# Optimization experiments

Measured on AMD Instinct MI355X. Metric: run time of the kernel, lower is better.

The kernel has to match this reference:

```python
import jax, jax.numpy as jnp
import numpy as np

B, N, D, K, L, H, DFF = 2048, 64, 256, 32, 2, 8, 1024
TEMP = 10.0
EPS = 1e-10


def _ln(x, g, b):
    m = jnp.mean(x, -1, keepdims=True)
    v = jnp.mean((x - m) ** 2, -1, keepdims=True)
    return (x - m) * jax.lax.rsqrt(v + 1e-5) * g + b


def _mha(x, Wqkv, bqkv, Wo, bo):
    b, n, d = x.shape
    dh = d // H
    qkv = x @ Wqkv.T + bqkv                      # [b,n,3d]
    q, k, v = jnp.split(qkv, 3, axis=-1)
    q = q.reshape(b, n, H, dh)
    k = k.reshape(b, n, H, dh)
    v = v.reshape(b, n, H, dh)
    att = jnp.einsum('bqhd,bkhd->bhqk', q, k) / np.float32(np.sqrt(dh))
    att = jax.nn.softmax(att, axis=-1)
    o = jnp.einsum('bhqk,bkhd->bqhd', att, v).reshape(b, n, d)
    return o @ Wo.T + bo


def _encoder(x, Wqkv, bqkv, Wo, bo, ln1_g, ln1_b, ln2_g, ln2_b, W1, b1, W2, b2):
    # torch TransformerEncoder, norm_first=False (post-LN), dropout=0
    for l in range(L):
        x = _ln(x + _mha(x, Wqkv[l], bqkv[l], Wo[l], bo[l]), ln1_g[l], ln1_b[l])
        h = jax.nn.relu(x @ W1[l].T + b1[l]) @ W2[l].T + b2[l]
        x = _ln(x + h, ln2_g[l], ln2_b[l])
    return x


def _cluster_probs_from_emb(emb, mus):
    # ||x - tanh(mu)||^2 via expansion to avoid the [B,N,K,D] intermediate
    mt = jnp.tanh(mus)                                       # [K,D]
    d2 = (jnp.sum(emb ** 2, -1)[..., None]
          - 2.0 * jnp.einsum('bnd,kd->bnk', emb, mt)
          + jnp.sum(mt ** 2, -1))                            # [B,N,K]
    e = jnp.exp(-d2 / TEMP)
    return e / jnp.sum(e, -1, keepdims=True)


def _forward(input_series, init_logits, transition_logits,
             Wqkv, bqkv, Wo, bo, ln1_g, ln1_b, ln2_g, ln2_b,
             W1, b1, W2, b2, mus):
    prob_pi = jax.nn.softmax(init_logits, axis=0)            # [K]
    prob_A = jax.nn.softmax(transition_logits, axis=1)       # [K,K]
    emb_all = _encoder(input_series, Wqkv, bqkv, Wo, bo,
                       ln1_g, ln1_b, ln2_g, ln2_b, W1, b1, W2, b2)
    logits_all = _cluster_probs_from_emb(emb_all, mus)       # [B,N,K]

    log_emit = jnp.log(logits_all + EPS)                     # [B,N,K]
    lt0 = jax.nn.softmax(jnp.log(prob_pi + EPS)[None, :] + log_emit[:, 0], axis=1)

    def step(lt, le):
        lt = jax.nn.softmax(jnp.log(lt @ prob_A + EPS) + le, axis=1)
        return lt, lt

    _, rest = jax.lax.scan(step, lt0, jnp.swapaxes(log_emit[:, 1:], 0, 1))
    cluster_probs = jnp.concatenate([lt0[:, None], jnp.swapaxes(rest, 0, 1)], axis=1)
    entropy_loss = -jnp.mean(jnp.sum(cluster_probs * jnp.log(cluster_probs + EPS), -1))
    return cluster_probs, emb_all, prob_pi, prob_A, entropy_loss


def setup_inputs() -> dict:
    key = jax.random.key(0)
    ks = jax.random.split(key, 10)
    s = jnp.float32(0.02)
    return {
        'input_series': jax.random.normal(ks[0], (B, N, D), jnp.float32),
        'init_logits': jax.random.normal(ks[1], (K,), jnp.float32),
        'transition_logits': jax.random.normal(ks[2], (K, K), jnp.float32),
        'Wqkv': jax.random.normal(ks[3], (L, 3 * D, D), jnp.float32) * s,
        'bqkv': jnp.zeros((L, 3 * D), jnp.float32),
        'Wo': jax.random.normal(ks[4], (L, D, D), jnp.float32) * s,
        'bo': jnp.zeros((L, D), jnp.float32),
        'ln1_g': jnp.ones((L, D), jnp.float32),
        'ln1_b': jnp.zeros((L, D), jnp.float32),
        'ln2_g': jnp.ones((L, D), jnp.float32),
        'ln2_b': jnp.zeros((L, D), jnp.float32),
        'W1': jax.random.normal(ks[5], (L, DFF, D), jnp.float32) * s,
        'b1': jnp.zeros((L, DFF), jnp.float32),
        'W2': jax.random.normal(ks[6], (L, D, DFF), jnp.float32) * s,
        'b2': jnp.zeros((L, D), jnp.float32),
        'mus': jax.random.normal(ks[7], (K, D), jnp.float32),
    }


def reference(input_series, init_logits, transition_logits, Wqkv, bqkv, Wo, bo,
              ln1_g, ln1_b, ln2_g, ln2_b, W1, b1, W2, b2, mus):
    return _forward(input_series, init_logits, transition_logits, Wqkv, bqkv,
                    Wo, bo, ln1_g, ln1_b, ln2_g, ln2_b, W1, b1, W2, b2, mus)
```

## Files before the change

kernel.cpp:

```cpp
#include <hip/hip_runtime.h>

#define BB   2048
#define NNX  64
#define DD   256
#define KKC  32
#define LLN  2
#define HHN  8
#define DHH  32
#define DFFN 1024
#define BNT  (BB*NNX)

typedef short s16x8 __attribute__((ext_vector_type(8)));
typedef float f32x4 __attribute__((ext_vector_type(4)));

#define GLOAD_LDS16(gp, lp) __builtin_amdgcn_global_load_lds( \
    (const __attribute__((address_space(1))) void*)(gp),      \
    (__attribute__((address_space(3))) void*)(lp), 16, 0, 0)

#define WAITVM4() asm volatile("s_waitcnt vmcnt(4)" ::: "memory")
#define WAITVM0() asm volatile("s_waitcnt vmcnt(0)" ::: "memory")
#define WAITLGKM0() do { asm volatile("s_waitcnt lgkmcnt(0)" ::: "memory"); \
                         __builtin_amdgcn_sched_barrier(0); } while (0)
#define SBAR() __builtin_amdgcn_s_barrier()

__device__ __forceinline__ unsigned short f2bf(float f) {
  unsigned int u = __float_as_uint(f);
  u += 0x7fffu + ((u >> 16) & 1u);
  return (unsigned short)(u >> 16);
}
__device__ __forceinline__ float bf2f(unsigned short u) {
  return __uint_as_float(((unsigned int)u) << 16);
}

__device__ __forceinline__ unsigned char f2fp8(float f) {
  unsigned u = __float_as_uint(f);
  unsigned lsb = (u >> 20) & 1u;
  u += 0x7FFFFu + lsb;
  int e = (int)((u >> 23) & 255u) - 120;
  if (e <= 0) {
    int q = (int)(f * 512.f + 0.5f);
    return (unsigned char)q;
  }
  if (e > 15) return 0x7E;
  return (unsigned char)((e << 3) | ((u >> 20) & 7u));
}
__device__ __forceinline__ unsigned char f2fp8s(float f) {
  unsigned s = __float_as_uint(f) >> 31;
  float a = fminf(fabsf(f), 448.f);
  return (unsigned char)((s << 7) | f2fp8(a));
}
__device__ __forceinline__ unsigned char p2fp8(float f) {
  unsigned u = __float_as_uint(f);
  u += 0x7FFFFu + ((u >> 20) & 1u);
  int e = (int)((u >> 23) & 255u) - 120;
  if (e <= 0) return 0;
  return (unsigned char)((e << 3) | ((u >> 20) & 7u));
}

__global__ __launch_bounds__(256) void cvt_kernel(const float4* __restrict__ src,
                                                  ushort4* __restrict__ dst, int n4) {
  int i = blockIdx.x * 256 + threadIdx.x;
  int st = gridDim.x * 256;
  for (; i < n4; i += st) {
    float4 v = src[i];
    ushort4 o;
    o.x = f2bf(v.x); o.y = f2bf(v.y); o.z = f2bf(v.z); o.w = f2bf(v.w);
    dst[i] = o;
  }
}

__global__ __launch_bounds__(256) void cvtw_kernel(const float4* __restrict__ wq, ushort4* __restrict__ dq,
                                                   const float4* __restrict__ wo, ushort4* __restrict__ dov,
                                                   const float4* __restrict__ w1, ushort4* __restrict__ d1,
                                                   const float4* __restrict__ w2, uchar4* __restrict__ d2,
                                                   const float* __restrict__ mus, unsigned short* __restrict__ mtb,
                                                   float* __restrict__ mtn,
                                                   const float* __restrict__ il, const float* __restrict__ tl,
                                                   float* __restrict__ d_pi, float* __restrict__ d_A,
                                                   float* __restrict__ d_ent) {
  if (blockIdx.x >= 512) {
    int lane = threadIdx.x;
    if (blockIdx.x == 512) {
      if (lane < 32) {
        float acc = 0.f;
        for (int d = 0; d < 256; d++) {
          float t = tanhf(mus[lane * 256 + d]);
          mtb[lane * 264 + d] = f2bf(t);
          acc += t * t;
        }
        mtn[lane] = acc;
      }
    } else {
      if (lane == 0) *d_ent = 0.f;
      if (lane < 32) {
        float v = il[lane];
        float mx = v;
        #pragma unroll
        for (int off = 16; off; off >>= 1) mx = fmaxf(mx, __shfl_xor(mx, off, 32));
        float e = expf(v - mx), sm = e;
        #pragma unroll
        for (int off = 16; off; off >>= 1) sm += __shfl_xor(sm, off, 32);
        d_pi[lane] = e / sm;
        for (int r = 0; r < 32; r++) {
          float a = tl[r * 32 + lane];
          float m2 = a;
          #pragma unroll
          for (int off = 16; off; off >>= 1) m2 = fmaxf(m2, __shfl_xor(m2, off, 32));
          float e2 = expf(a - m2), s2 = e2;
          #pragma unroll
          for (int off = 16; off; off >>= 1) s2 += __shfl_xor(s2, off, 32);
          d_A[r * 32 + lane] = e2 / s2;
        }
      }
    }
    return;
  }
  const int n0 = 98304, n1 = 32768, n2 = 131072, n3 = 131072;
  int i = blockIdx.x * 256 + threadIdx.x;
  int st = 512 * 256;
  for (; i < n0 + n1 + n2 + n3; i += st) {
    int j = i;
    if (j < n0) {
      float4 v = wq[j];
      dq[j] = (ushort4){f2bf(v.x), f2bf(v.y), f2bf(v.z), f2bf(v.w)};
    } else if ((j -= n0) < n1) {
      float4 v = wo[j];
      dov[j] = (ushort4){f2bf(v.x), f2bf(v.y), f2bf(v.z), f2bf(v.w)};
    } else if ((j -= n1) < n2) {
      float4 v = w1[j];
      d1[j] = (ushort4){f2bf(v.x), f2bf(v.y), f2bf(v.z), f2bf(v.w)};
    } else {
      j -= n2;
      float4 v = w2[j];
      d2[j] = (uchar4){f2fp8s(v.x * 64.f), f2fp8s(v.y * 64.f),
                       f2fp8s(v.z * 64.f), f2fp8s(v.w * 64.f)};
    }
  }
}

template <int EPI>
__global__ __launch_bounds__(256, 4) void gemm_nt(const unsigned short* __restrict__ A,
                                                  const unsigned short* __restrict__ Bw,
                                                  const float* __restrict__ bias,
                                                  void* __restrict__ outp,
                                                  int N, int K, int nx) {
  __shared__ unsigned short lds[16384];
  const int t = threadIdx.x;
  const int bid = blockIdx.x, nwg = gridDim.x;
  const int wg = (bid & 7) * (nwg >> 3) + (bid >> 3);
  const int m0 = (wg / nx) << 7;
  const int n0 = (wg % nx) << 7;
  const int lane = t & 63, w = t >> 6;
  const int wm = w >> 1, wn = w & 1;
  const int lr = lane & 15, lk = lane >> 4;

  const int r0 = t >> 2, sg = t & 3;
  const int s0 = sg ^ ((r0 >> 1) & 3);
  const int r1 = r0 + 64;
  const int s1 = sg ^ ((r1 >> 1) & 3);
  const int aoff0 = (m0 + r0) * K + s0 * 8;
  const int aoff1 = (m0 + r1) * K + s1 * 8;
  const int boff0 = (n0 + r0) * K + s0 * 8;
  const int boff1 = (n0 + r1) * K + s1 * 8;

#define STAGE(buf, k0) do {                                    \
    char* la = (char*)lds + (buf) * 16384;                     \
    GLOAD_LDS16(A + aoff0 + (k0), la + t * 16);                \
    GLOAD_LDS16(A + aoff1 + (k0), la + 4096 + t * 16);         \
    GLOAD_LDS16(Bw + boff0 + (k0), la + 8192 + t * 16);        \
    GLOAD_LDS16(Bw + boff1 + (k0), la + 12288 + t * 16);       \
  } while (0)

  f32x4 acc[4][4];
  #pragma unroll
  for (int i = 0; i < 4; i++)
    #pragma unroll
    for (int j = 0; j < 4; j++) acc[i][j] = (f32x4)(0.f);

  const int ra = wm * 64 + lr, rb = wn * 64 + lr;
  const int sla = lk ^ ((ra >> 1) & 3), slb = lk ^ ((rb >> 1) & 3);

  const int NT = K >> 5;
  STAGE(0, 0);
  STAGE(1, 32);
  WAITVM4();
  SBAR();

  int c = 0;
  for (int kt = 0; kt < NT; kt++) {
    s16x8 af[4], bf[4];
    {
      const unsigned short* ua = lds + c * 8192;
      const unsigned short* ub = ua + 4096;
      #pragma unroll
      for (int mf = 0; mf < 4; mf++)
        af[mf] = *(const s16x8*)&ua[(ra + mf * 16) * 32 + sla * 8];
      #pragma unroll
      for (int nf = 0; nf < 4; nf++)
        bf[nf] = *(const s16x8*)&ub[(rb + nf * 16) * 32 + slb * 8];
    }
    __builtin_amdgcn_s_setprio(1);
    #pragma unroll
    for (int mf = 0; mf < 4; mf++)
      #pragma unroll
      for (int nf = 0; nf < 4; nf++)
        acc[mf][nf] = __builtin_amdgcn_mfma_f32_16x16x32_bf16(af[mf], bf[nf], acc[mf][nf], 0, 0, 0);
    __builtin_amdgcn_s_setprio(0);
    SBAR();
    if (kt < NT - 2) {
      STAGE(c, (kt + 2) << 5);
      WAITVM4();
    } else if (kt == NT - 2) {
      WAITVM0();
    }
    SBAR();
    c ^= 1;
  }
#undef STAGE

  #pragma unroll
  for (int nf = 0; nf < 4; nf++) {
    int col = n0 + wn * 64 + nf * 16 + lr;
    float bv = bias[col];
    #pragma unroll
    for (int mf = 0; mf < 4; mf++)
      #pragma unroll
      for (int r = 0; r < 4; r++) {
        int row = m0 + wm * 64 + mf * 16 + lk * 4 + r;
        size_t o = (size_t)row * N + col;
        float v = acc[mf][nf][r] + bv;
        if (EPI == 0) {
          ((unsigned short*)outp)[o] = f2bf(v);
        } else if (EPI == 1) {
          float hh = fminf(fmaxf(v, 0.f) * 8.f, 448.f);
          ((unsigned char*)outp)[o] = f2fp8(hh);
        } else {
          ((unsigned char*)outp)[o] = f2fp8s(v * 32.f);
        }
      }
  }
}

template <bool WR32>
__global__ __launch_bounds__(512) void gemm_ln(const unsigned short* __restrict__ A,
                                               const unsigned short* __restrict__ Bw,
                                               const float* __restrict__ bias,
                                               const unsigned short* __restrict__ res,
                                               const float* __restrict__ g,
                                               const float* __restrict__ bta,
                                               unsigned short* __restrict__ xb,
                                               float* __restrict__ x32,
                                               int K) {
  __shared__ unsigned short As[128 * 64];
  __shared__ unsigned short Bs[256 * 64];
  __shared__ float stats[2][128][4];
  const int t = threadIdx.x;
  const int nwg = gridDim.x;
  const int bid = blockIdx.x;
  const int wg = (bid & 7) * (nwg >> 3) + (bid >> 3);
  const int m0 = wg << 7;

  const int lane = t & 63, w = t >> 6;
  const int wm = w >> 2, wn = w & 3;
  const int lr = lane & 15, lk = lane >> 4;

  size_t aoff[2], boff[4];
  #pragma unroll
  for (int p = 0; p < 2; p++) {
    int u = p * 512 + t;
    int row = u >> 3, sp = u & 7;
    int seg = sp ^ (((row >> 2) & 1) << 1);
    aoff[p] = (size_t)(m0 + row) * K + seg * 8;
  }
  #pragma unroll
  for (int p = 0; p < 4; p++) {
    int u = p * 512 + t;
    int row = u >> 3, sp = u & 7;
    int seg = sp ^ (((row >> 2) & 1) << 1);
    boff[p] = (size_t)row * K + seg * 8;
  }

  f32x4 acc[4][4];
  #pragma unroll
  for (int i = 0; i < 4; i++)
    #pragma unroll
    for (int j = 0; j < 4; j++) acc[i][j] = (f32x4)(0.f);

  for (int k0 = 0; k0 < K; k0 += 64) {
    #pragma unroll
    for (int p = 0; p < 2; p++)
      GLOAD_LDS16(A + aoff[p] + k0, (char*)As + (p * 512 + t) * 16);
    #pragma unroll
    for (int p = 0; p < 4; p++)
      GLOAD_LDS16(Bw + boff[p] + k0, (char*)Bs + (p * 512 + t) * 16);
    __syncthreads();
    #pragma unroll
    for (int z = 0; z < 2; z++) {
      s16x8 af[4], bfr[4];
      #pragma unroll
      for (int mf = 0; mf < 4; mf++) {
        int row = wm * 64 + mf * 16 + lr;
        int cc = (z * 4 + lk) ^ (((row >> 2) & 1) << 1);
        af[mf] = *(const s16x8*)&As[row * 64 + cc * 8];
      }
      #pragma unroll
      for (int nf = 0; nf < 4; nf++) {
        int row = wn * 64 + nf * 16 + lr;
        int cc = (z * 4 + lk) ^ (((row >> 2) & 1) << 1);
        bfr[nf] = *(const s16x8*)&Bs[row * 64 + cc * 8];
      }
      #pragma unroll
      for (int mf = 0; mf < 4; mf++)
        #pragma unroll
        for (int nf = 0; nf < 4; nf++)
          acc[mf][nf] = __builtin_amdgcn_mfma_f32_16x16x32_bf16(af[mf], bfr[nf], acc[mf][nf], 0, 0, 0);
    }
    __syncthreads();
  }

  float bv[4];
  #pragma unroll
  for (int nf = 0; nf < 4; nf++) bv[nf] = bias[wn * 64 + nf * 16 + lr];

  #pragma unroll
  for (int mf = 0; mf < 4; mf++) {
    #pragma unroll
    for (int r = 0; r < 4; r++) {
      int grow = m0 + wm * 64 + mf * 16 + lk * 4 + r;
      float s = 0.f, q = 0.f;
      #pragma unroll
      for (int nf = 0; nf < 4; nf++) {
        int col = wn * 64 + nf * 16 + lr;
        float v = acc[mf][nf][r] + bv[nf] + bf2f(res[(size_t)grow * 256 + col]);
        acc[mf][nf][r] = v;
        s += v; q += v * v;
      }
      #pragma unroll
      for (int off = 1; off < 16; off <<= 1) { s += __shfl_xor(s, off); q += __shfl_xor(q, off); }
      if (lr == 0) {
        int lrow = wm * 64 + mf * 16 + lk * 4 + r;
        stats[0][lrow][wn] = s;
        stats[1][lrow][wn] = q;
      }
    }
  }
  __syncthreads();

  float gv[4], bbv[4];
  #pragma unroll
  for (int nf = 0; nf < 4; nf++) {
    int col = wn * 64 + nf * 16 + lr;
    gv[nf] = g[col]; bbv[nf] = bta[col];
  }
  #pragma unroll
  for (int mf = 0; mf < 4; mf++) {
    #pragma unroll
    for (int r = 0; r < 4; r++) {
      int lrow = wm * 64 + mf * 16 + lk * 4 + r;
      int grow = m0 + lrow;
      float s4 = stats[0][lrow][0] + stats[0][lrow][1] + stats[0][lrow][2] + stats[0][lrow][3];
      float q4 = stats[1][lrow][0] + stats[1][lrow][1] + stats[1][lrow][2] + stats[1][lrow][3];
      float mean = s4 * (1.f / 256.f);
      float var = q4 * (1.f / 256.f) - mean * mean;
      float rs = rsqrtf(var + 1e-5f);
      #pragma unroll
      for (int nf = 0; nf < 4; nf++) {
        int col = wn * 64 + nf * 16 + lr;
        float val = (acc[mf][nf][r] - mean) * rs * gv[nf] + bbv[nf];
        xb[(size_t)grow * 256 + col] = f2bf(val);
        if (WR32) x32[(size_t)grow * 256 + col] = val;
      }
    }
  }
}

template <bool WR32>
__global__ __launch_bounds__(512) void gemm_ln_fp8(const unsigned char* __restrict__ A,
                                                   const unsigned char* __restrict__ Bw,
                                                   const float* __restrict__ bias,
                                                   const unsigned short* __restrict__ res,
                                                   const float* __restrict__ g,
                                                   const float* __restrict__ bta,
                                                   unsigned short* __restrict__ xb,
                                                   float* __restrict__ x32,
                                                   int K) {
  __shared__ unsigned char lds8[24576];
  float* stats = (float*)lds8;
  const int t = threadIdx.x;
  const int nwg = gridDim.x;
  const int bid = blockIdx.x;
  const int wg = (bid & 7) * (nwg >> 3) + (bid >> 3);
  const int m0 = wg << 7;

  const int lane = t & 63, w = t >> 6;
  const int wm = w >> 2, wn = w & 3;
  const int lr = lane & 15, lk = lane >> 4;

  const int auu = t >> 8, arow = (t >> 1) & 127, asg = t & 1;
  const size_t aoff = (size_t)(m0 + arow) * K + auu * 32 + asg * 16;
  size_t boff[2];
  #pragma unroll
  for (int p = 0; p < 2; p++) {
    int idx = p * 512 + t;
    int buu = idx >> 9, brow = (idx >> 1) & 255, bsg = idx & 1;
    boff[p] = (size_t)brow * K + buu * 32 + bsg * 16;
  }

  f32x4 acc[4][4];
  #pragma unroll
  for (int i = 0; i < 4; i++)
    #pragma unroll
    for (int j = 0; j < 4; j++) acc[i][j] = (f32x4)(0.f);

  for (int k0 = 0; k0 < K; k0 += 64) {
    GLOAD_LDS16(A + aoff + k0, (char*)lds8 + t * 16);
    GLOAD_LDS16(Bw + boff[0] + k0, (char*)lds8 + 8192 + t * 16);
    GLOAD_LDS16(Bw + boff[1] + k0, (char*)lds8 + 16384 + t * 16);
    __syncthreads();
    #pragma unroll
    for (int kk = 0; kk < 2; kk++) {
      long long af[4], bf[4];
      #pragma unroll
      for (int mf = 0; mf < 4; mf++)
        af[mf] = *(const long long*)&lds8[kk * 4096 + (wm * 64 + mf * 16 + lr) * 32 + lk * 8];
      #pragma unroll
      for (int nf = 0; nf < 4; nf++)
        bf[nf] = *(const long long*)&lds8[8192 + kk * 8192 + (wn * 64 + nf * 16 + lr) * 32 + lk * 8];
      #pragma unroll
      for (int mf = 0; mf < 4; mf++)
        #pragma unroll
        for (int nf = 0; nf < 4; nf++)
          acc[mf][nf] = __builtin_amdgcn_mfma_f32_16x16x32_fp8_fp8(af[mf], bf[nf], acc[mf][nf], 0, 0, 0);
    }
    __syncthreads();
  }

  const float isc = 1.f / 512.f;
  float bv[4];
  #pragma unroll
  for (int nf = 0; nf < 4; nf++) bv[nf] = bias[wn * 64 + nf * 16 + lr];

  #pragma unroll
  for (int mf = 0; mf < 4; mf++) {
    #pragma unroll
    for (int r = 0; r < 4; r++) {
      int grow = m0 + wm * 64 + mf * 16 + lk * 4 + r;
      float s = 0.f, q = 0.f;
      #pragma unroll
      for (int nf = 0; nf < 4; nf++) {
        int col = wn * 64 + nf * 16 + lr;
        float v = acc[mf][nf][r] * isc + bv[nf] + bf2f(res[(size_t)grow * 256 + col]);
        acc[mf][nf][r] = v;
        s += v; q += v * v;
      }
      #pragma unroll
      for (int off = 1; off < 16; off <<= 1) { s += __shfl_xor(s, off); q += __shfl_xor(q, off); }
      if (lr == 0) {
        int lrow = wm * 64 + mf * 16 + lk * 4 + r;
        stats[lrow * 4 + wn] = s;
        stats[512 + lrow * 4 + wn] = q;
      }
    }
  }
  __syncthreads();

  float gv[4], bbv[4];
  #pragma unroll
  for (int nf = 0; nf < 4; nf++) {
    int col = wn * 64 + nf * 16 + lr;
    gv[nf] = g[col]; bbv[nf] = bta[col];
  }
  #pragma unroll
  for (int mf = 0; mf < 4; mf++) {
    #pragma unroll
    for (int r = 0; r < 4; r++) {
      int lrow = wm * 64 + mf * 16 + lk * 4 + r;
      int grow = m0 + lrow;
      float s4 = stats[lrow * 4 + 0] + stats[lrow * 4 + 1] + stats[lrow * 4 + 2] + stats[lrow * 4 + 3];
      float q4 = stats[512 + lrow * 4 + 0] + stats[512 + lrow * 4 + 1]
               + stats[512 + lrow * 4 + 2] + stats[512 + lrow * 4 + 3];
      float mean = s4 * (1.f / 256.f);
      float var = q4 * (1.f / 256.f) - mean * mean;
      float rs = rsqrtf(var + 1e-5f);
      #pragma unroll
      for (int nf = 0; nf < 4; nf++) {
        int col = wn * 64 + nf * 16 + lr;
        float val = (acc[mf][nf][r] - mean) * rs * gv[nf] + bbv[nf];
        xb[(size_t)grow * 256 + col] = f2bf(val);
        if (WR32) x32[(size_t)grow * 256 + col] = val;
      }
    }
  }
}

__global__ __launch_bounds__(256) void attn_kernel(const unsigned char* __restrict__ qkv,
                                                   unsigned short* __restrict__ ob) {
  __shared__ unsigned char al[28672];
  const int wv = threadIdx.x >> 6;
  unsigned char* wb = al + wv * 7168;
  unsigned char* qs = wb;
  unsigned char* ks = wb + 2048;
  unsigned char* vs = wb + 4096;
  unsigned char* vt = wb;
  unsigned char* ps = wb + 2304;
  const int bh = blockIdx.x * 4 + wv;
  const int b = bh >> 3, h = bh & 7;
  const int lane = threadIdx.x & 63;
  const int lr = lane & 15, lk = lane >> 4;

  #pragma unroll
  for (int p = 0; p < 2; p++) {
    int u = lane + p * 64;
    int row = u >> 1, seg = u & 1;
    size_t gb = (size_t)(b * 64 + row) * 768 + h * 32 + seg * 16;
    GLOAD_LDS16(qkv + gb, (char*)wb + u * 16);
    GLOAD_LDS16(qkv + gb + 256, (char*)wb + 2048 + u * 16);
    GLOAD_LDS16(qkv + gb + 512, (char*)wb + 4096 + u * 16);
  }
  __syncthreads();

  long long aq[4], bk[4], vchunk[4];
  #pragma unroll
  for (int mi = 0; mi < 4; mi++)
    aq[mi] = *(const long long*)&qs[(mi * 16 + lr) * 32 + lk * 8];
  #pragma unroll
  for (int nj = 0; nj < 4; nj++)
    bk[nj] = *(const long long*)&ks[(nj * 16 + lr) * 32 + lk * 8];
  const int vrow = lane >> 2, vcs = (lane & 3) * 8;
  #pragma unroll
  for (int q = 0; q < 4; q++)
    vchunk[q] = *(const long long*)&vs[(q * 16 + vrow) * 32 + vcs];
  WAITLGKM0();

  #pragma unroll
  for (int q = 0; q < 4; q++) {
    unsigned long long vv = (unsigned long long)vchunk[q];
    #pragma unroll
    for (int j = 0; j < 8; j++)
      vt[(vcs + j) * 72 + q * 16 + vrow] = (unsigned char)(vv >> (8 * j));
  }

  f32x4 s[4][4];
  #pragma unroll
  for (int i = 0; i < 4; i++)
    #pragma unroll
    for (int j = 0; j < 4; j++) s[i][j] = (f32x4)(0.f);
  #pragma unroll
  for (int mi = 0; mi < 4; mi++)
    #pragma unroll
    for (int nj = 0; nj < 4; nj++)
      s[mi][nj] = __builtin_amdgcn_mfma_f32_16x16x32_fp8_fp8(aq[mi], bk[nj], s[mi][nj], 0, 0, 0);

  const float scale = 0.17677669529663687f / 1024.f;
  #pragma unroll
  for (int mi = 0; mi < 4; mi++) {
    #pragma unroll
    for (int r = 0; r < 4; r++) {
      float t0 = s[mi][0][r] * scale, t1 = s[mi][1][r] * scale;
      float t2 = s[mi][2][r] * scale, t3 = s[mi][3][r] * scale;
      float mx = fmaxf(fmaxf(t0, t1), fmaxf(t2, t3));
      #pragma unroll
      for (int off = 8; off; off >>= 1) mx = fmaxf(mx, __shfl_xor(mx, off, 16));
      float e0 = expf(t0 - mx), e1 = expf(t1 - mx), e2 = expf(t2 - mx), e3 = expf(t3 - mx);
      float sm = e0 + e1 + e2 + e3;
      #pragma unroll
      for (int off = 8; off; off >>= 1) sm += __shfl_xor(sm, off, 16);
      float inv = 128.f / sm;
      int prow = mi * 16 + lk * 4 + r;
      ps[prow * 72 + lr + 0]  = p2fp8(e0 * inv);
      ps[prow * 72 + lr + 16] = p2fp8(e1 * inv);
      ps[prow * 72 + lr + 32] = p2fp8(e2 * inv);
      ps[prow * 72 + lr + 48] = p2fp8(e3 * inv);
    }
  }
  WAITLGKM0();

  f32x4 oacc[4][2];
  #pragma unroll
  for (int i = 0; i < 4; i++) { oacc[i][0] = (f32x4)(0.f); oacc[i][1] = (f32x4)(0.f); }
  #pragma unroll
  for (int kk = 0; kk < 2; kk++) {
    long long bv[2];
    #pragma unroll
    for (int nf = 0; nf < 2; nf++)
      bv[nf] = *(const long long*)&vt[(nf * 16 + lr) * 72 + kk * 32 + lk * 8];
    #pragma unroll
    for (int mi = 0; mi < 4; mi++) {
      long long ap = *(const long long*)&ps[(mi * 16 + lr) * 72 + kk * 32 + lk * 8];
      #pragma unroll
      for (int nf = 0; nf < 2; nf++)
        oacc[mi][nf] = __builtin_amdgcn_mfma_f32_16x16x32_fp8_fp8(ap, bv[nf], oacc[mi][nf], 0, 0, 0);
    }
  }
  const float osc = 1.f / 4096.f;
  #pragma unroll
  for (int mi = 0; mi < 4; mi++)
    #pragma unroll
    for (int nf = 0; nf < 2; nf++)
      #pragma unroll
      for (int r = 0; r < 4; r++) {
        int tok = mi * 16 + lk * 4 + r;
        int c = nf * 16 + lr;
        ob[(size_t)(b * 64 + tok) * 256 + h * 32 + c] = f2bf(oacc[mi][nf][r] * osc);
      }
}

__global__ __launch_bounds__(256) void cluster_scan_kernel(const unsigned short* __restrict__ xb,
                                                           const unsigned short* __restrict__ mtb,
                                                           const float* __restrict__ mtn,
                                                           const float* __restrict__ pi,
                                                           const float* __restrict__ Atr,
                                                           float* __restrict__ cp,
                                                           float* __restrict__ ent) {
  __shared__ unsigned short ms[32 * 264];
  __shared__ float les[4][64][32];
  const int t = threadIdx.x;
  for (int i = t; i < 2112; i += 256)
    ((uint2*)ms)[i] = ((const uint2*)mtb)[i];
  const int lane = t & 63, w = t >> 6;
  const int lr = lane & 15, lk = lane >> 4;
  const float mtn0 = mtn[lr], mtn1 = mtn[16 + lr];
  __syncthreads();

  const size_t tok0 = (size_t)blockIdx.x * 256 + (size_t)w * 64;
  f32x4 s[4][2];
  #pragma unroll
  for (int i = 0; i < 4; i++) { s[i][0] = (f32x4)(0.f); s[i][1] = (f32x4)(0.f); }

  #pragma unroll
  for (int kk = 0; kk < 8; kk++) {
    s16x8 bf0 = *(const s16x8*)&ms[lr * 264 + lk * 8 + kk * 32];
    s16x8 bf1 = *(const s16x8*)&ms[(16 + lr) * 264 + lk * 8 + kk * 32];
    #pragma unroll
    for (int mi = 0; mi < 4; mi++) {
      s16x8 af = *(const s16x8*)&xb[(tok0 + mi * 16 + lr) * 256 + lk * 8 + kk * 32];
      s[mi][0] = __builtin_amdgcn_mfma_f32_16x16x32_bf16(af, bf0, s[mi][0], 0, 0, 0);
      s[mi][1] = __builtin_amdgcn_mfma_f32_16x16x32_bf16(af, bf1, s[mi][1], 0, 0, 0);
    }
  }

  #pragma unroll
  for (int mi = 0; mi < 4; mi++) {
    #pragma unroll
    for (int r = 0; r < 4; r++) {
      float l0 = (2.f * s[mi][0][r] - mtn0) * 0.1f;
      float l1 = (2.f * s[mi][1][r] - mtn1) * 0.1f;
      float mx = fmaxf(l0, l1);
      #pragma unroll
      for (int off = 8; off; off >>= 1) mx = fmaxf(mx, __shfl_xor(mx, off, 16));
      float e0 = expf(l0 - mx), e1 = expf(l1 - mx);
      float sm = e0 + e1;
      #pragma unroll
      for (int off = 8; off; off >>= 1) sm += __shfl_xor(sm, off, 16);
      float inv = 1.f / sm;
      int row = mi * 16 + lk * 4 + r;
      les[w][row][lr]      = logf(e0 * inv + 1e-10f);
      les[w][row][16 + lr] = logf(e1 * inv + 1e-10f);
    }
  }

  if (lane < 32) {
    const int j = lane;
    const int batch = blockIdx.x * 4 + w;
    float regA[32];
    #pragma unroll
    for (int i = 0; i < 32; i++) regA[i] = Atr[i * 32 + j];
    float* cpo = cp + (size_t)batch * 64 * 32;

    float u = logf(pi[j] + 1e-10f) + les[w][0][j];
    float mx = u;
    #pragma unroll
    for (int off = 16; off; off >>= 1) mx = fmaxf(mx, __shfl_xor(mx, off, 32));
    float e = expf(u - mx), sm = e;
    #pragma unroll
    for (int off = 16; off; off >>= 1) sm += __shfl_xor(sm, off, 32);
    float p = e / sm;
    cpo[j] = p;
    float enta = p * logf(p + 1e-10f);

    for (int n = 1; n < 64; n++) {
      float tt = 0.f;
      #pragma unroll
      for (int i = 0; i < 32; i++) tt += __shfl(p, i, 32) * regA[i];
      u = logf(tt + 1e-10f) + les[w][n][j];
      mx = u;
      #pragma unroll
      for (int off = 16; off; off >>= 1) mx = fmaxf(mx, __shfl_xor(mx, off, 32));
      e = expf(u - mx); sm = e;
      #pragma unroll
      for (int off = 16; off; off >>= 1) sm += __shfl_xor(sm, off, 32);
      p = e / sm;
      cpo[n * 32 + j] = p;
      enta += p * logf(p + 1e-10f);
    }
    #pragma unroll
    for (int off = 16; off; off >>= 1) enta += __shfl_xor(enta, off, 32);
    if (j == 0) atomicAdd(ent, -enta * (1.f / (2048.f * 64.f)));
  }
}

extern "C" void kernel_launch(void* const* d_in, const int* in_sizes, int n_in,
                              void* d_out, int out_size, void* d_ws, size_t ws_size,
                              hipStream_t stream) {
  const float* input = (const float*)d_in[0];
  const float* init_logits = (const float*)d_in[1];
  const float* trans = (const float*)d_in[2];
  const float* Wqkv = (const float*)d_in[3];
  const float* bqkv = (const float*)d_in[4];
  const float* Wo = (const float*)d_in[5];
  const float* bo = (const float*)d_in[6];
  const float* ln1g = (const float*)d_in[7];
  const float* ln1b = (const float*)d_in[8];
  const float* ln2g = (const float*)d_in[9];
  const float* ln2b = (const float*)d_in[10];
  const float* W1 = (const float*)d_in[11];
  const float* b1 = (const float*)d_in[12];
  const float* W2 = (const float*)d_in[13];
  const float* b2 = (const float*)d_in[14];
  const float* mus = (const float*)d_in[15];

  float* out = (float*)d_out;
  float* cp = out;
  float* x = out + 4194304;
  float* d_pi = out + 37748736;
  float* d_A = out + 37748768;
  float* d_ent = out + 37749792;

  char* ws = (char*)d_ws;
  unsigned char* qkv = (unsigned char*)ws;
  unsigned char* hb = (unsigned char*)ws;
  unsigned short* ob = (unsigned short*)(ws + 268435456ull);
  unsigned short* xb = (unsigned short*)(ws + 335544320ull);
  unsigned short* wq_b = (unsigned short*)(ws + 402653184ull);
  unsigned short* wo_b = (unsigned short*)(ws + 402653184ull + 786432ull);
  unsigned short* w1_b = (unsigned short*)(ws + 402653184ull + 1048576ull);
  unsigned char* w2_f = (unsigned char*)(ws + 402653184ull + 2097152ull);
  unsigned short* mtb = (unsigned short*)(ws + 402653184ull + 3145728ull);
  float* mtn = (float*)(ws + 402653184ull + 3178496ull);

  cvt_kernel<<<2048, 256, 0, stream>>>((const float4*)input, (ushort4*)xb, BNT * 256 / 4);
  cvtw_kernel<<<514, 256, 0, stream>>>((const float4*)Wqkv, (ushort4*)wq_b,
                                       (const float4*)Wo, (ushort4*)wo_b,
                                       (const float4*)W1, (ushort4*)w1_b,
                                       (const float4*)W2, (uchar4*)w2_f,
                                       mus, mtb, mtn,
                                       init_logits, trans, d_pi, d_A, d_ent);

  for (int l = 0; l < 2; l++) {
    gemm_nt<2><<<6144, 256, 0, stream>>>(xb, wq_b + l * 196608, bqkv + l * 768,
                                         qkv, 768, 256, 6);
    attn_kernel<<<4096, 256, 0, stream>>>(qkv, ob);
    gemm_ln<false><<<1024, 512, 0, stream>>>(ob, wo_b + l * 65536, bo + l * 256,
                                             xb, ln1g + l * 256, ln1b + l * 256,
                                             xb, nullptr, 256);
    gemm_nt<1><<<8192, 256, 0, stream>>>(xb, w1_b + l * 262144, b1 + l * 1024,
                                         hb, 1024, 256, 8);
    if (l == LLN - 1)
      gemm_ln_fp8<true><<<1024, 512, 0, stream>>>(hb, w2_f + l * 262144, b2 + l * 256,
                                                  xb, ln2g + l * 256, ln2b + l * 256,
                                                  xb, x, 1024);
    else
      gemm_ln_fp8<false><<<1024, 512, 0, stream>>>(hb, w2_f + l * 262144, b2 + l * 256,
                                                   xb, ln2g + l * 256, ln2b + l * 256,
                                                   xb, nullptr, 1024);
  }

  cluster_scan_kernel<<<512, 256, 0, stream>>>(xb, mtb, mtn, d_pi, d_A, cp, d_ent);
}
```

Measured before the change: 1.060 ms.

## Fuse FFN up and down projections into one fp8 kernel with LayerNorm

Combines the W1 GEMM, ReLU, W2 GEMM and the second LayerNorm into a single kernel. The 64-row hidden chunks stay in shared memory instead of being written to and read back from global memory. W1 and the post-attention activations are now quantized to scaled fp8, so the first GEMM also runs on fp8 MFMA, and gemm_ln writes an extra fp8 copy of x. The fused loop reloads the weights for each chunk with a full wait and barrier and has no double buffering, so memory latency is exposed, and the extra fp8 quantization lowers accuracy.

```diff
diff --git a/kernel.cpp b/kernel.cpp
--- a/kernel.cpp
+++ b/kernel.cpp
@@ -71,7 +71,7 @@
 
 __global__ __launch_bounds__(256) void cvtw_kernel(const float4* __restrict__ wq, ushort4* __restrict__ dq,
                                                    const float4* __restrict__ wo, ushort4* __restrict__ dov,
-                                                   const float4* __restrict__ w1, ushort4* __restrict__ d1,
+                                                   const float4* __restrict__ w1, uchar4* __restrict__ d1,
                                                    const float4* __restrict__ w2, uchar4* __restrict__ d2,
                                                    const float* __restrict__ mus, unsigned short* __restrict__ mtb,
                                                    float* __restrict__ mtn,
@@ -128,7 +128,8 @@
       dov[j] = (ushort4){f2bf(v.x), f2bf(v.y), f2bf(v.z), f2bf(v.w)};
     } else if ((j -= n1) < n2) {
       float4 v = w1[j];
-      d1[j] = (ushort4){f2bf(v.x), f2bf(v.y), f2bf(v.z), f2bf(v.w)};
+      d1[j] = (uchar4){f2fp8s(v.x * 64.f), f2fp8s(v.y * 64.f),
+                       f2fp8s(v.z * 64.f), f2fp8s(v.w * 64.f)};
     } else {
       j -= n2;
       float4 v = w2[j];
@@ -231,9 +232,6 @@
         float v = acc[mf][nf][r] + bv;
         if (EPI == 0) {
           ((unsigned short*)outp)[o] = f2bf(v);
-        } else if (EPI == 1) {
-          float hh = fminf(fmaxf(v, 0.f) * 8.f, 448.f);
-          ((unsigned char*)outp)[o] = f2fp8(hh);
         } else {
           ((unsigned char*)outp)[o] = f2fp8s(v * 32.f);
         }
@@ -241,7 +239,6 @@
   }
 }
 
-template <bool WR32>
 __global__ __launch_bounds__(512) void gemm_ln(const unsigned short* __restrict__ A,
                                                const unsigned short* __restrict__ Bw,
                                                const float* __restrict__ bias,
@@ -249,7 +246,7 @@
                                                const float* __restrict__ g,
                                                const float* __restrict__ bta,
                                                unsigned short* __restrict__ xb,
-                                               float* __restrict__ x32,
+                                               unsigned char* __restrict__ xb8,
                                                int K) {
   __shared__ unsigned short As[128 * 64];
   __shared__ unsigned short Bs[256 * 64];
@@ -367,44 +364,63 @@
       for (int nf = 0; nf < 4; nf++) {
         int col = wn * 64 + nf * 16 + lr;
         float val = (acc[mf][nf][r] - mean) * rs * gv[nf] + bbv[nf];
-        xb[(size_t)grow * 256 + col] = f2bf(val);
-        if (WR32) x32[(size_t)grow * 256 + col] = val;
+        size_t o = (size_t)grow * 256 + col;
+        xb[o] = f2bf(val);
+        xb8[o] = f2fp8s(val * 32.f);
       }
     }
   }
 }
 
 template <bool WR32>
-__global__ __launch_bounds__(512) void gemm_ln_fp8(const unsigned char* __restrict__ A,
-                                                   const unsigned char* __restrict__ Bw,
-                                                   const float* __restrict__ bias,
+__global__ __launch_bounds__(256, 2) void gemm_ffn(const unsigned char* __restrict__ x8,
+                                                   const unsigned char* __restrict__ w1f,
+                                                   const unsigned char* __restrict__ w2f,
+                                                   const float* __restrict__ b1,
+                                                   const float* __restrict__ b2,
                                                    const unsigned short* __restrict__ res,
                                                    const float* __restrict__ g,
                                                    const float* __restrict__ bta,
                                                    unsigned short* __restrict__ xb,
-                                                   float* __restrict__ x32,
-                                                   int K) {
-  __shared__ unsigned char lds8[24576];
+                                                   float* __restrict__ x32) {
+  __shared__ unsigned char lds8[53760];
   float* stats = (float*)lds8;
   const int t = threadIdx.x;
-  const int nwg = gridDim.x;
-  const int bid = blockIdx.x;
+  const int bid = blockIdx.x, nwg = gridDim.x;
   const int wg = (bid & 7) * (nwg >> 3) + (bid >> 3);
-  const int m0 = wg << 7;
-
-  const int lane = t & 63, w = t >> 6;
-  const int wm = w >> 2, wn = w & 3;
+  const int m0 = wg << 6;
+  const int lane = t & 63, wv = t >> 6;
   const int lr = lane & 15, lk = lane >> 4;
 
-  const int auu = t >> 8, arow = (t >> 1) & 127, asg = t & 1;
-  const size_t aoff = (size_t)(m0 + arow) * K + auu * 32 + asg * 16;
-  size_t boff[2];
-  #pragma unroll
-  for (int p = 0; p < 2; p++) {
-    int idx = p * 512 + t;
-    int buu = idx >> 9, brow = (idx >> 1) & 255, bsg = idx & 1;
-    boff[p] = (size_t)brow * K + buu * 32 + bsg * 16;
-  }
+  const int xu = t >> 7, xrow = (t >> 1) & 63, xsg = t & 1;
+
+  #pragma unroll
+  for (int p = 0; p < 4; p++) {
+    int idx = p * 256 + t;
+    int u = idx >> 7, row = (idx >> 1) & 63, sgg = idx & 1;
+    GLOAD_LDS16(x8 + (size_t)(m0 + row) * 256 + u * 32 + sgg * 16, (char*)lds8 + idx * 16);
+  }
+
+#define STAGE_W(c) do {                                                          \
+    _Pragma("unroll")                                                            \
+    for (int p = 0; p < 4; p++) {                                                \
+      int idx = p * 256 + t;                                                     \
+      int u = idx >> 7, row = (idx >> 1) & 63, sgg = idx & 1;                    \
+      GLOAD_LDS16(w1f + (size_t)((c) * 64 + row) * 256 + u * 32 + sgg * 16,      \
+                  (char*)lds8 + 16384 + idx * 16);                               \
+    }                                                                            \
+    _Pragma("unroll")                                                            \
+    for (int p = 0; p < 4; p++) {                                                \
+      int idx = p * 256 + t;                                                     \
+      int u = idx >> 9, row = (idx >> 1) & 255, sgg = idx & 1;                   \
+      GLOAD_LDS16(w2f + (size_t)row * 1024 + (c) * 64 + u * 32 + sgg * 16,       \
+                  (char*)lds8 + 32768 + idx * 16);                               \
+    }                                                                            \
+  } while (0)
+
+  STAGE_W(0);
+  WAITVM0();
+  SBAR();
 
   f32x4 acc[4][4];
   #pragma unroll
@@ -412,54 +428,77 @@
     #pragma unroll
     for (int j = 0; j < 4; j++) acc[i][j] = (f32x4)(0.f);
 
-  for (int k0 = 0; k0 < K; k0 += 64) {
-    GLOAD_LDS16(A + aoff + k0, (char*)lds8 + t * 16);
-    GLOAD_LDS16(Bw + boff[0] + k0, (char*)lds8 + 8192 + t * 16);
-    GLOAD_LDS16(Bw + boff[1] + k0, (char*)lds8 + 16384 + t * 16);
-    __syncthreads();
-    #pragma unroll
-    for (int kk = 0; kk < 2; kk++) {
-      long long af[4], bf[4];
-      #pragma unroll
-      for (int mf = 0; mf < 4; mf++)
-        af[mf] = *(const long long*)&lds8[kk * 4096 + (wm * 64 + mf * 16 + lr) * 32 + lk * 8];
-      #pragma unroll
-      for (int nf = 0; nf < 4; nf++)
-        bf[nf] = *(const long long*)&lds8[8192 + kk * 8192 + (wn * 64 + nf * 16 + lr) * 32 + lk * 8];
+  for (int c = 0; c < 16; c++) {
+    f32x4 hacc[4];
+    #pragma unroll
+    for (int i = 0; i < 4; i++) hacc[i] = (f32x4)(0.f);
+    #pragma unroll
+    for (int kk = 0; kk < 8; kk++) {
+      long long bf1 = *(const long long*)&lds8[16384 + kk * 2048 + (wv * 16 + lr) * 32 + lk * 8];
+      #pragma unroll
+      for (int mf = 0; mf < 4; mf++) {
+        long long af = *(const long long*)&lds8[kk * 2048 + (mf * 16 + lr) * 32 + lk * 8];
+        hacc[mf] = __builtin_amdgcn_mfma_f32_16x16x32_fp8_fp8(af, bf1, hacc[mf], 0, 0, 0);
+      }
+    }
+    {
+      float b1v = b1[c * 64 + wv * 16 + lr];
       #pragma unroll
       for (int mf = 0; mf < 4; mf++)
         #pragma unroll
+        for (int r = 0; r < 4; r++) {
+          float hv = hacc[mf][r] * (1.f / 2048.f) + b1v;
+          hv = fminf(fmaxf(hv, 0.f) * 8.f, 448.f);
+          lds8[49152 + (mf * 16 + lk * 4 + r) * 72 + wv * 16 + lr] = f2fp8(hv);
+        }
+    }
+    SBAR();
+    #pragma unroll
+    for (int kk2 = 0; kk2 < 2; kk2++) {
+      long long bf2[4];
+      #pragma unroll
+      for (int nf = 0; nf < 4; nf++)
+        bf2[nf] = *(const long long*)&lds8[32768 + kk2 * 8192 + (wv * 64 + nf * 16 + lr) * 32 + lk * 8];
+      #pragma unroll
+      for (int mf = 0; mf < 4; mf++) {
+        long long af2 = *(const long long*)&lds8[49152 + (mf * 16 + lr) * 72 + kk2 * 32 + lk * 8];
+        #pragma unroll
         for (int nf = 0; nf < 4; nf++)
-          acc[mf][nf] = __builtin_amdgcn_mfma_f32_16x16x32_fp8_fp8(af[mf], bf[nf], acc[mf][nf], 0, 0, 0);
-    }
-    __syncthreads();
-  }
-
+          acc[mf][nf] = __builtin_amdgcn_mfma_f32_16x16x32_fp8_fp8(af2, bf2[nf], acc[mf][nf], 0, 0, 0);
+      }
+    }
+    SBAR();
+    if (c < 15) {
+      STAGE_W(c + 1);
+      WAITVM0();
+      SBAR();
+    }
+  }
+#undef STAGE_W
+
+  __syncthreads();
   const float isc = 1.f / 512.f;
   float bv[4];
   #pragma unroll
-  for (int nf = 0; nf < 4; nf++) bv[nf] = bias[wn * 64 + nf * 16 + lr];
+  for (int nf = 0; nf < 4; nf++) bv[nf] = b2[wv * 64 + nf * 16 + lr];
 
   #pragma unroll
   for (int mf = 0; mf < 4; mf++) {
     #pragma unroll
     for (int r = 0; r < 4; r++) {
-      int grow = m0 + wm * 64 + mf * 16 + lk * 4 + r;
+      int lrow = mf * 16 + lk * 4 + r;
+      int grow = m0 + lrow;
       float s = 0.f, q = 0.f;
       #pragma unroll
       for (int nf = 0; nf < 4; nf++) {
-        int col = wn * 64 + nf * 16 + lr;
+        int col = wv * 64 + nf * 16 + lr;
         float v = acc[mf][nf][r] * isc + bv[nf] + bf2f(res[(size_t)grow * 256 + col]);
         acc[mf][nf][r] = v;
         s += v; q += v * v;
       }
       #pragma unroll
       for (int off = 1; off < 16; off <<= 1) { s += __shfl_xor(s, off); q += __shfl_xor(q, off); }
-      if (lr == 0) {
-        int lrow = wm * 64 + mf * 16 + lk * 4 + r;
-        stats[lrow * 4 + wn] = s;
-        stats[512 + lrow * 4 + wn] = q;
-      }
+      if (lr == 0) { stats[lrow * 4 + wv] = s; stats[256 + lrow * 4 + wv] = q; }
     }
   }
   __syncthreads();
@@ -467,24 +506,24 @@
   float gv[4], bbv[4];
   #pragma unroll
   for (int nf = 0; nf < 4; nf++) {
-    int col = wn * 64 + nf * 16 + lr;
+    int col = wv * 64 + nf * 16 + lr;
     gv[nf] = g[col]; bbv[nf] = bta[col];
   }
   #pragma unroll
   for (int mf = 0; mf < 4; mf++) {
     #pragma unroll
     for (int r = 0; r < 4; r++) {
-      int lrow = wm * 64 + mf * 16 + lk * 4 + r;
+      int lrow = mf * 16 + lk * 4 + r;
       int grow = m0 + lrow;
       float s4 = stats[lrow * 4 + 0] + stats[lrow * 4 + 1] + stats[lrow * 4 + 2] + stats[lrow * 4 + 3];
-      float q4 = stats[512 + lrow * 4 + 0] + stats[512 + lrow * 4 + 1]
-               + stats[512 + lrow * 4 + 2] + stats[512 + lrow * 4 + 3];
+      float q4 = stats[256 + lrow * 4 + 0] + stats[256 + lrow * 4 + 1]
+               + stats[256 + lrow * 4 + 2] + stats[256 + lrow * 4 + 3];
       float mean = s4 * (1.f / 256.f);
       float var = q4 * (1.f / 256.f) - mean * mean;
       float rs = rsqrtf(var + 1e-5f);
       #pragma unroll
       for (int nf = 0; nf < 4; nf++) {
-        int col = wn * 64 + nf * 16 + lr;
+        int col = wv * 64 + nf * 16 + lr;
         float val = (acc[mf][nf][r] - mean) * rs * gv[nf] + bbv[nf];
         xb[(size_t)grow * 256 + col] = f2bf(val);
         if (WR32) x32[(size_t)grow * 256 + col] = val;
@@ -728,12 +767,12 @@
 
   char* ws = (char*)d_ws;
   unsigned char* qkv = (unsigned char*)ws;
-  unsigned char* hb = (unsigned char*)ws;
+  unsigned char* xb8 = (unsigned char*)(ws + 134217728ull);
   unsigned short* ob = (unsigned short*)(ws + 268435456ull);
   unsigned short* xb = (unsigned short*)(ws + 335544320ull);
   unsigned short* wq_b = (unsigned short*)(ws + 402653184ull);
   unsigned short* wo_b = (unsigned short*)(ws + 402653184ull + 786432ull);
-  unsigned short* w1_b = (unsigned short*)(ws + 402653184ull + 1048576ull);
+  unsigned char* w1_f = (unsigned char*)(ws + 402653184ull + 1048576ull);
   unsigned char* w2_f = (unsigned char*)(ws + 402653184ull + 2097152ull);
   unsigned short* mtb = (unsigned short*)(ws + 402653184ull + 3145728ull);
   float* mtn = (float*)(ws + 402653184ull + 3178496ull);
@@ -741,7 +780,7 @@
   cvt_kernel<<<2048, 256, 0, stream>>>((const float4*)input, (ushort4*)xb, BNT * 256 / 4);
   cvtw_kernel<<<514, 256, 0, stream>>>((const float4*)Wqkv, (ushort4*)wq_b,
                                        (const float4*)Wo, (ushort4*)wo_b,
-                                       (const float4*)W1, (ushort4*)w1_b,
+                                       (const float4*)W1, (uchar4*)w1_f,
                                        (const float4*)W2, (uchar4*)w2_f,
                                        mus, mtb, mtn,
                                        init_logits, trans, d_pi, d_A, d_ent);
@@ -750,19 +789,19 @@
     gemm_nt<2><<<6144, 256, 0, stream>>>(xb, wq_b + l * 196608, bqkv + l * 768,
                                          qkv, 768, 256, 6);
     attn_kernel<<<4096, 256, 0, stream>>>(qkv, ob);
-    gemm_ln<false><<<1024, 512, 0, stream>>>(ob, wo_b + l * 65536, bo + l * 256,
-                                             xb, ln1g + l * 256, ln1b + l * 256,
-                                             xb, nullptr, 256);
-    gemm_nt<1><<<8192, 256, 0, stream>>>(xb, w1_b + l * 262144, b1 + l * 1024,
-                                         hb, 1024, 256, 8);
+    gemm_ln<<<1024, 512, 0, stream>>>(ob, wo_b + l * 65536, bo + l * 256,
+                                      xb, ln1g + l * 256, ln1b + l * 256,
+                                      xb, xb8, 256);
     if (l == LLN - 1)
-      gemm_ln_fp8<true><<<1024, 512, 0, stream>>>(hb, w2_f + l * 262144, b2 + l * 256,
-                                                  xb, ln2g + l * 256, ln2b + l * 256,
-                                                  xb, x, 1024);
+      gemm_ffn<true><<<2048, 256, 0, stream>>>(xb8, w1_f + l * 262144, w2_f + l * 262144,
+                                               b1 + l * 1024, b2 + l * 256,
+                                               xb, ln2g + l * 256, ln2b + l * 256,
+                                               xb, x);
     else
-      gemm_ln_fp8<false><<<1024, 512, 0, stream>>>(hb, w2_f + l * 262144, b2 + l * 256,
-                                                   xb, ln2g + l * 256, ln2b + l * 256,
-                                                   xb, nullptr, 1024);
+      gemm_ffn<false><<<2048, 256, 0, stream>>>(xb8, w1_f + l * 262144, w2_f + l * 262144,
+                                                b1 + l * 1024, b2 + l * 256,
+                                                xb, ln2g + l * 256, ln2b + l * 256,
+                                                xb, nullptr);
   }
 
   cluster_scan_kernel<<<512, 256, 0, stream>>>(xb, mtb, mtn, d_pi, d_A, cp, d_ent);
```

Result: slower. 1.138 ms (+7.3%).

## Run the FFN up-projection GEMM in FP8 with a new 128x256-tile kernel

Applied to the files above, without the earlier changes.

W1 is now quantized to scaled FP8 instead of bf16. The attention-output LayerNorm kernel additionally writes an FP8 copy of the activations. A new gemm_h_fp8 kernel computes the FFN up-projection with fp8 MFMA on 128x256 tiles, replacing the bf16 gemm_nt path. This halves operand bytes and uses the higher-throughput fp8 matrix instructions, but adds an extra activation write and reduces precision in the FFN input.

```diff
diff --git a/kernel.cpp b/kernel.cpp
--- a/kernel.cpp
+++ b/kernel.cpp
@@ -71,7 +71,7 @@
 
 __global__ __launch_bounds__(256) void cvtw_kernel(const float4* __restrict__ wq, ushort4* __restrict__ dq,
                                                    const float4* __restrict__ wo, ushort4* __restrict__ dov,
-                                                   const float4* __restrict__ w1, ushort4* __restrict__ d1,
+                                                   const float4* __restrict__ w1, uchar4* __restrict__ d1,
                                                    const float4* __restrict__ w2, uchar4* __restrict__ d2,
                                                    const float* __restrict__ mus, unsigned short* __restrict__ mtb,
                                                    float* __restrict__ mtn,
@@ -128,7 +128,8 @@
       dov[j] = (ushort4){f2bf(v.x), f2bf(v.y), f2bf(v.z), f2bf(v.w)};
     } else if ((j -= n1) < n2) {
       float4 v = w1[j];
-      d1[j] = (ushort4){f2bf(v.x), f2bf(v.y), f2bf(v.z), f2bf(v.w)};
+      d1[j] = (uchar4){f2fp8s(v.x * 64.f), f2fp8s(v.y * 64.f),
+                       f2fp8s(v.z * 64.f), f2fp8s(v.w * 64.f)};
     } else {
       j -= n2;
       float4 v = w2[j];
@@ -231,9 +232,6 @@
         float v = acc[mf][nf][r] + bv;
         if (EPI == 0) {
           ((unsigned short*)outp)[o] = f2bf(v);
-        } else if (EPI == 1) {
-          float hh = fminf(fmaxf(v, 0.f) * 8.f, 448.f);
-          ((unsigned char*)outp)[o] = f2fp8(hh);
         } else {
           ((unsigned char*)outp)[o] = f2fp8s(v * 32.f);
         }
@@ -241,7 +239,6 @@
   }
 }
 
-template <bool WR32>
 __global__ __launch_bounds__(512) void gemm_ln(const unsigned short* __restrict__ A,
                                                const unsigned short* __restrict__ Bw,
                                                const float* __restrict__ bias,
@@ -249,7 +246,7 @@
                                                const float* __restrict__ g,
                                                const float* __restrict__ bta,
                                                unsigned short* __restrict__ xb,
-                                               float* __restrict__ x32,
+                                               unsigned char* __restrict__ xb8,
                                                int K) {
   __shared__ unsigned short As[128 * 64];
   __shared__ unsigned short Bs[256 * 64];
@@ -367,10 +364,84 @@
       for (int nf = 0; nf < 4; nf++) {
         int col = wn * 64 + nf * 16 + lr;
         float val = (acc[mf][nf][r] - mean) * rs * gv[nf] + bbv[nf];
-        xb[(size_t)grow * 256 + col] = f2bf(val);
-        if (WR32) x32[(size_t)grow * 256 + col] = val;
-      }
-    }
+        size_t o = (size_t)grow * 256 + col;
+        xb[o] = f2bf(val);
+        xb8[o] = f2fp8s(val * 32.f);
+      }
+    }
+  }
+}
+
+__global__ __launch_bounds__(512) void gemm_h_fp8(const unsigned char* __restrict__ A,
+                                                  const unsigned char* __restrict__ Bw,
+                                                  const float* __restrict__ bias,
+                                                  unsigned char* __restrict__ outp,
+                                                  int nx) {
+  __shared__ unsigned char lds8[24576];
+  const int t = threadIdx.x;
+  const int bid = blockIdx.x, nwg = gridDim.x;
+  const int wg = (bid & 7) * (nwg >> 3) + (bid >> 3);
+  const int m0 = (wg / nx) << 7;
+  const int n0 = (wg % nx) << 8;
+  const int K = 256;
+
+  const int lane = t & 63, w = t >> 6;
+  const int wm = w >> 2, wn = w & 3;
+  const int lr = lane & 15, lk = lane >> 4;
+
+  const int auu = t >> 8, arow = (t >> 1) & 127, asg = t & 1;
+  const size_t aoff = (size_t)(m0 + arow) * K + auu * 32 + asg * 16;
+  size_t boff[2];
+  #pragma unroll
+  for (int p = 0; p < 2; p++) {
+    int idx = p * 512 + t;
+    int buu = idx >> 9, brow = (idx >> 1) & 255, bsg = idx & 1;
+    boff[p] = (size_t)(n0 + brow) * K + buu * 32 + bsg * 16;
+  }
+
+  f32x4 acc[4][4];
+  #pragma unroll
+  for (int i = 0; i < 4; i++)
+    #pragma unroll
+    for (int j = 0; j < 4; j++) acc[i][j] = (f32x4)(0.f);
+
+  for (int k0 = 0; k0 < K; k0 += 64) {
+    GLOAD_LDS16(A + aoff + k0, (char*)lds8 + t * 16);
+    GLOAD_LDS16(Bw + boff[0] + k0, (char*)lds8 + 8192 + t * 16);
+    GLOAD_LDS16(Bw + boff[1] + k0, (char*)lds8 + 16384 + t * 16);
+    __syncthreads();
+    #pragma unroll
+    for (int kk = 0; kk < 2; kk++) {
+      long long af[4], bf[4];
+      #pragma unroll
+      for (int mf = 0; mf < 4; mf++)
+        af[mf] = *(const long long*)&lds8[kk * 4096 + (wm * 64 + mf * 16 + lr) * 32 + lk * 8];
+      #pragma unroll
+      for (int nf = 0; nf < 4; nf++)
+        bf[nf] = *(const long long*)&lds8[8192 + kk * 8192 + (wn * 64 + nf * 16 + lr) * 32 + lk * 8];
+      #pragma unroll
+      for (int mf = 0; mf < 4; mf++)
+        #pragma unroll
+        for (int nf = 0; nf < 4; nf++)
+          acc[mf][nf] = __builtin_amdgcn_mfma_f32_16x16x32_fp8_fp8(af[mf], bf[nf], acc[mf][nf], 0, 0, 0);
+    }
+    __syncthreads();
+  }
+
+  const float isc = 1.f / 2048.f;
+  #pragma unroll
+  for (int nf = 0; nf < 4; nf++) {
+    int col = n0 + wn * 64 + nf * 16 + lr;
+    float bv = bias[col];
+    #pragma unroll
+    for (int mf = 0; mf < 4; mf++)
+      #pragma unroll
+      for (int r = 0; r < 4; r++) {
+        int row = m0 + wm * 64 + mf * 16 + lk * 4 + r;
+        float v = acc[mf][nf][r] * isc + bv;
+        float hh = fminf(fmaxf(v, 0.f) * 8.f, 448.f);
+        outp[(size_t)row * 1024 + col] = f2fp8(hh);
+      }
   }
 }
 
@@ -729,11 +800,12 @@
   char* ws = (char*)d_ws;
   unsigned char* qkv = (unsigned char*)ws;
   unsigned char* hb = (unsigned char*)ws;
+  unsigned char* xb8 = (unsigned char*)(ws + 134217728ull);
   unsigned short* ob = (unsigned short*)(ws + 268435456ull);
   unsigned short* xb = (unsigned short*)(ws + 335544320ull);
   unsigned short* wq_b = (unsigned short*)(ws + 402653184ull);
   unsigned short* wo_b = (unsigned short*)(ws + 402653184ull + 786432ull);
-  unsigned short* w1_b = (unsigned short*)(ws + 402653184ull + 1048576ull);
+  unsigned char* w1_f = (unsigned char*)(ws + 402653184ull + 1048576ull);
   unsigned char* w2_f = (unsigned char*)(ws + 402653184ull + 2097152ull);
   unsigned short* mtb = (unsigned short*)(ws + 402653184ull + 3145728ull);
   float* mtn = (float*)(ws + 402653184ull + 3178496ull);
@@ -741,7 +813,7 @@
   cvt_kernel<<<2048, 256, 0, stream>>>((const float4*)input, (ushort4*)xb, BNT * 256 / 4);
   cvtw_kernel<<<514, 256, 0, stream>>>((const float4*)Wqkv, (ushort4*)wq_b,
                                        (const float4*)Wo, (ushort4*)wo_b,
-                                       (const float4*)W1, (ushort4*)w1_b,
+                                       (const float4*)W1, (uchar4*)w1_f,
                                        (const float4*)W2, (uchar4*)w2_f,
                                        mus, mtb, mtn,
                                        init_logits, trans, d_pi, d_A, d_ent);
@@ -750,11 +822,11 @@
     gemm_nt<2><<<6144, 256, 0, stream>>>(xb, wq_b + l * 196608, bqkv + l * 768,
                                          qkv, 768, 256, 6);
     attn_kernel<<<4096, 256, 0, stream>>>(qkv, ob);
-    gemm_ln<false><<<1024, 512, 0, stream>>>(ob, wo_b + l * 65536, bo + l * 256,
-                                             xb, ln1g + l * 256, ln1b + l * 256,
-                                             xb, nullptr, 256);
-    gemm_nt<1><<<8192, 256, 0, stream>>>(xb, w1_b + l * 262144, b1 + l * 1024,
-                                         hb, 1024, 256, 8);
+    gemm_ln<<<1024, 512, 0, stream>>>(ob, wo_b + l * 65536, bo + l * 256,
+                                      xb, ln1g + l * 256, ln1b + l * 256,
+                                      xb, xb8, 256);
+    gemm_h_fp8<<<4096, 512, 0, stream>>>(xb8, w1_f + l * 262144, b1 + l * 1024,
+                                         hb, 4);
     if (l == LLN - 1)
       gemm_ln_fp8<true><<<1024, 512, 0, stream>>>(hb, w2_f + l * 262144, b2 + l * 256,
                                                   xb, ln2g + l * 256, ln2b + l * 256,
```

Result: slower. 1.133 ms (+6.9%).
